# Performance work log

Hardware: AMD Instinct MI355X
Metric: run time of the kernel (lower is better)

Reference implementation:

```python
import jax, jax.numpy as jnp
import numpy as np

N = 100000
E = 800000
F_IN = 64
HID = 128


def setup_inputs() -> dict:
    key = jax.random.key(0)
    ks = jax.random.split(key, 10)
    x = jax.random.normal(ks[0], (N, F_IN), dtype=jnp.float32)
    edge_index = jax.random.randint(ks[1], (2, E), 0, N, dtype=jnp.int64)
    s = 0.05
    # PyG GraphConv: lin_rel (with bias) applied to aggregated neighbors, lin_root (no bias) to self
    return {
        "x": x,
        "edge_index": edge_index,
        "W1_rel": jax.random.normal(ks[2], (HID, F_IN), dtype=jnp.float32) * s,
        "b1": jnp.zeros((HID,), dtype=jnp.float32),
        "W1_root": jax.random.normal(ks[3], (HID, F_IN), dtype=jnp.float32) * s,
        "W2_rel": jax.random.normal(ks[4], (HID, HID), dtype=jnp.float32) * s,
        "b2": jnp.zeros((HID,), dtype=jnp.float32),
        "W2_root": jax.random.normal(ks[5], (HID, HID), dtype=jnp.float32) * s,
        "W_fc1": jax.random.normal(ks[6], (20, HID), dtype=jnp.float32) * s,
        "b_fc1": jnp.zeros((20,), dtype=jnp.float32),
        "W_fc2": jax.random.normal(ks[7], (1, 20), dtype=jnp.float32) * s,
        "b_fc2": jnp.zeros((1,), dtype=jnp.float32),
    }


def graph_conv(x, edge_index, W_rel, b_rel, W_root):
    # sum-aggregate source features onto destination nodes (PyG GraphConv, aggr='add')
    src, dst = edge_index[0], edge_index[1]
    agg = jax.ops.segment_sum(x[src], dst, num_segments=N)  # [N, F]
    return agg @ W_rel.T + b_rel + x @ W_root.T


def reference(x, edge_index, W1_rel, b1, W1_root, W2_rel, b2, W2_root,
              W_fc1, b_fc1, W_fc2, b_fc2):
    h = graph_conv(x, edge_index, W1_rel, b1, W1_root)
    h = jax.nn.elu(h)
    h = graph_conv(h, edge_index, W2_rel, b2, W2_root)
    h = jax.nn.relu(h @ W_fc1.T + b_fc1)
    out = h @ W_fc2.T + b_fc2  # [N, 1]
    return out
```

## Files before the change

### kernel.cpp

```cpp
#include <hip/hip_runtime.h>

#define N_NODES 100000
#define N_EDGES 800000
#define FIN 64
#define HID 128
#define NB1 391
#define SRCS_CAP (N_EDGES + 3 * N_NODES)
#define GI (1024 * 256)

typedef unsigned short ushort_t;
typedef __attribute__((ext_vector_type(8))) short short8;
typedef __attribute__((ext_vector_type(16))) float fx16;
typedef __attribute__((ext_vector_type(4))) unsigned short us4;

__device__ inline ushort_t f2bf(float f) {
    unsigned u = __float_as_uint(f);
    u += 0x7fffu + ((u >> 16) & 1u);
    return (ushort_t)(u >> 16);
}

__device__ inline void upadd(float* acc, uint4 A) {
    acc[0] += __uint_as_float(A.x << 16);
    acc[1] += __uint_as_float(A.x & 0xffff0000u);
    acc[2] += __uint_as_float(A.y << 16);
    acc[3] += __uint_as_float(A.y & 0xffff0000u);
    acc[4] += __uint_as_float(A.z << 16);
    acc[5] += __uint_as_float(A.z & 0xffff0000u);
    acc[6] += __uint_as_float(A.w << 16);
    acc[7] += __uint_as_float(A.w & 0xffff0000u);
}

__global__ __launch_bounds__(256) void init_kernel(
    const int* __restrict__ ei, const float* __restrict__ x,
    const float* __restrict__ W1rel, const float* __restrict__ W1root,
    const float* __restrict__ W2rel, const float* __restrict__ W2root,
    const float* __restrict__ b2, const float* __restrict__ Wfc1,
    const float* __restrict__ bfc1, const float* __restrict__ Wfc2,
    int* __restrict__ deg, int* __restrict__ flag, int* __restrict__ srcs,
    ushort_t* __restrict__ xb, ushort_t* __restrict__ Wb1,
    ushort_t* __restrict__ Mb, float* __restrict__ cbp, float* __restrict__ w2p) {
    __shared__ int s[256];
    int t = threadIdx.x;
    int gtid = blockIdx.x * 256 + t;

    if (gtid < N_NODES) deg[gtid] = 0;
    for (int k = gtid; k < SRCS_CAP; k += GI) srcs[k] = N_NODES;
    for (int i = gtid; i < N_NODES * FIN / 4; i += GI) {
        float4 v = ((const float4*)x)[i];
        us4 o = {f2bf(v.x), f2bf(v.y), f2bf(v.z), f2bf(v.w)};
        ((us4*)xb)[i] = o;
    }
    us4 z = {0, 0, 0, 0};
    if (gtid < 16) ((us4*)xb)[(size_t)N_NODES * 16 + gtid] = z;
    if (gtid < HID * HID) {
        int n = gtid >> 7, k = gtid & 127;
        float v = (k < FIN) ? W1rel[n * FIN + k] : W1root[n * FIN + (k - FIN)];
        Wb1[gtid] = f2bf(v);
    }
    if (blockIdx.x < 32) {
        int idx = blockIdx.x * 256 + t;
        int n = idx >> 7, k = idx & 127;
        float acc = 0.f;
        if (n < 20) {
            for (int j = 0; j < HID; j++) acc += Wfc1[n * HID + j] * W2rel[j * HID + k];
        } else if (n >= 32 && n < 52) {
            int m = n - 32;
            for (int j = 0; j < HID; j++) acc += Wfc1[m * HID + j] * W2root[j * HID + k];
        }
        Mb[idx] = f2bf(acc);
    }
    if (blockIdx.x == 32 && t < 32) {
        float cv = 0.f, wv = 0.f;
        if (t < 20) {
            for (int j = 0; j < HID; j++) cv += Wfc1[t * HID + j] * b2[j];
            cv += bfc1[t];
            wv = Wfc2[t];
        }
        cbp[t] = cv;
        w2p[t] = wv;
    }
    if (blockIdx.x == 33) {
        int bad = 0;
        for (int i = t; i < 8192; i += 256) bad |= ei[2 * i + 1];
        s[t] = bad;
        __syncthreads();
        for (int d = 128; d > 0; d >>= 1) {
            if (t < d) s[t] |= s[t + d];
            __syncthreads();
        }
        if (t == 0) *flag = (s[0] != 0) ? 1 : 0;
    }
}

__global__ void hist_kernel(const int* __restrict__ w, const int* __restrict__ flag,
                            int* __restrict__ deg) {
    int e = blockIdx.x * 256 + threadIdx.x;
    if (e >= N_EDGES) return;
    int is32 = *flag;
    int d = is32 ? w[N_EDGES + e] : w[2 * (N_EDGES + e)];
    atomicAdd(&deg[d], 1);
}

__global__ void scan1_kernel(const int* __restrict__ deg, int* __restrict__ off,
                             int* __restrict__ bsums) {
    __shared__ int s[256];
    int t = threadIdx.x;
    int i = blockIdx.x * 256 + t;
    int v = (i < N_NODES) ? ((deg[i] + 3) & ~3) : 0;
    s[t] = v;
    __syncthreads();
    for (int d = 1; d < 256; d <<= 1) {
        int w = (t >= d) ? s[t - d] : 0;
        __syncthreads();
        s[t] += w;
        __syncthreads();
    }
    if (i < N_NODES) off[i] = s[t] - v;
    if (t == 255) bsums[blockIdx.x] = s[255];
}

__global__ void scan23_kernel(int* __restrict__ off, const int* __restrict__ bsums,
                              int* __restrict__ cur) {
    __shared__ int s[256];
    int t = threadIdx.x, b = blockIdx.x;
    int pre = 0, tot = 0;
    for (int j = t; j < NB1; j += 256) {
        int v = bsums[j];
        if (j < b) pre += v;
        tot += v;
    }
    s[t] = pre;
    __syncthreads();
    for (int d = 128; d > 0; d >>= 1) {
        if (t < d) s[t] += s[t + d];
        __syncthreads();
    }
    int prefix = s[0];
    __syncthreads();
    int i = b * 256 + t;
    if (i < N_NODES) {
        int v = off[i] + prefix;
        off[i] = v;
        cur[i] = v;
    }
    if (b == 0) {
        s[t] = tot;
        __syncthreads();
        for (int d = 128; d > 0; d >>= 1) {
            if (t < d) s[t] += s[t + d];
            __syncthreads();
        }
        if (t == 0) off[N_NODES] = s[0];
    }
}

__global__ void scatter_kernel(const int* __restrict__ w, const int* __restrict__ flag,
                               int* __restrict__ cur, int* __restrict__ srcs) {
    int e = blockIdx.x * 256 + threadIdx.x;
    if (e >= N_EDGES) return;
    int is32 = *flag;
    int s = is32 ? w[e] : w[2 * e];
    int d = is32 ? w[N_EDGES + e] : w[2 * (N_EDGES + e)];
    int pos = atomicAdd(&cur[d], 1);
    srcs[pos] = s;
}

__global__ void agg1_kernel(const ushort_t* __restrict__ xb, const int* __restrict__ off,
                            const int* __restrict__ srcs, ushort_t* __restrict__ aggb) {
    int wid = (blockIdx.x * 256 + threadIdx.x) >> 6;
    int lane = threadIdx.x & 63;
    int n = lane >> 3;
    unsigned c = lane & 7;
    int node = wid * 8 + n;
    int b = off[node], e = off[node + 1];
    float acc[8];
#pragma unroll
    for (int j = 0; j < 8; j++) acc[j] = 0.f;
    const uint4* rows = (const uint4*)xb;
    for (int p = b; p < e; p += 4) {
        int4 s = *(const int4*)(srcs + p);
        uint4 A = rows[(unsigned)s.x * 8u + c];
        uint4 B = rows[(unsigned)s.y * 8u + c];
        uint4 C = rows[(unsigned)s.z * 8u + c];
        uint4 D = rows[(unsigned)s.w * 8u + c];
        upadd(acc, A);
        upadd(acc, B);
        upadd(acc, C);
        upadd(acc, D);
    }
    uint4 o = {(unsigned)f2bf(acc[0]) | ((unsigned)f2bf(acc[1]) << 16),
               (unsigned)f2bf(acc[2]) | ((unsigned)f2bf(acc[3]) << 16),
               (unsigned)f2bf(acc[4]) | ((unsigned)f2bf(acc[5]) << 16),
               (unsigned)f2bf(acc[6]) | ((unsigned)f2bf(acc[7]) << 16)};
    ((uint4*)(aggb + (size_t)node * FIN))[c] = o;
}

__global__ __launch_bounds__(256) void g12_kernel(
    const ushort_t* __restrict__ aggb, const ushort_t* __restrict__ xb,
    const ushort_t* __restrict__ Wb1, const float* __restrict__ b1,
    const ushort_t* __restrict__ Mb, ushort_t* __restrict__ uvb) {
    __shared__ ushort_t smem[24576];
    ushort_t* wl = smem;
    ushort_t* ml = smem + 16384;

    us4 z = {0, 0, 0, 0};
    if (blockIdx.x == 0 && threadIdx.x < 8)
        ((us4*)(uvb + (size_t)N_NODES * 64))[threadIdx.x] = z;

#pragma unroll
    for (int it = 0; it < 4; it++) {
        int q = it * 256 + threadIdx.x;
        int n = q >> 4, c = q & 15;
        short8 v = ((const short8*)Mb)[q];
        *(short8*)(ml + n * HID + ((c ^ (n & 7)) << 3)) = v;
    }
#pragma unroll
    for (int it = 0; it < 8; it++) {
        int q = it * 256 + threadIdx.x;
        int n = q >> 4, c = q & 15;
        short8 v = ((const short8*)Wb1)[q];
        *(short8*)(wl + n * HID + ((c ^ (n & 7)) << 3)) = v;
    }
    __syncthreads();

    int wave = threadIdx.x >> 6;
    int lane = threadIdx.x & 63;
    int half = lane >> 5, col = lane & 31;
    int nb = blockIdx.x * 128 + wave * 32;
    int nA = nb + col;
    if (nA >= N_NODES) nA = N_NODES - 1;

    short8 areg[8];
#pragma unroll
    for (int s = 0; s < 4; s++)
        areg[s] = *(const short8*)(aggb + (size_t)nA * FIN + s * 16 + half * 8);
#pragma unroll
    for (int s = 4; s < 8; s++)
        areg[s] = *(const short8*)(xb + (size_t)nA * FIN + (s - 4) * 16 + half * 8);

    fx16 acc[4];
#pragma unroll
    for (int jt = 0; jt < 4; jt++)
#pragma unroll
        for (int r = 0; r < 16; r++) acc[jt][r] = 0.f;

#pragma unroll
    for (int s = 0; s < 8; s++) {
        int c = 2 * s + half;
#pragma unroll
        for (int jt = 0; jt < 4; jt++) {
            int n = jt * 32 + col;
            short8 bq = *(const short8*)(wl + n * HID + ((c ^ (n & 7)) << 3));
            acc[jt] = __builtin_amdgcn_mfma_f32_32x32x16_bf16(areg[s], bq, acc[jt], 0, 0, 0);
        }
    }
    __syncthreads();

#pragma unroll
    for (int jt = 0; jt < 4; jt++) {
        int j = jt * 32 + col;
        float bias = b1[j];
#pragma unroll
        for (int r = 0; r < 16; r++) {
            int nl = wave * 32 + (r & 3) + 8 * (r >> 2) + 4 * half;
            float v = acc[jt][r] + bias;
            v = v > 0.f ? v : __expf(v) - 1.f;
            wl[nl * HID + (((j >> 3) ^ (nl & 7)) << 3) + (j & 7)] = f2bf(v);
        }
    }
    __syncthreads();

    int nl2 = wave * 32 + col;
    short8 af[8];
#pragma unroll
    for (int s = 0; s < 8; s++) {
        int c = 2 * s + half;
        af[s] = *(const short8*)(wl + nl2 * HID + ((c ^ (nl2 & 7)) << 3));
    }
    fx16 uacc[2];
#pragma unroll
    for (int jt = 0; jt < 2; jt++)
#pragma unroll
        for (int r = 0; r < 16; r++) uacc[jt][r] = 0.f;

#pragma unroll
    for (int s = 0; s < 8; s++) {
        int c = 2 * s + half;
#pragma unroll
        for (int jt = 0; jt < 2; jt++) {
            int n = jt * 32 + col;
            short8 bq = *(const short8*)(ml + n * HID + ((c ^ (n & 7)) << 3));
            uacc[jt] = __builtin_amdgcn_mfma_f32_32x32x16_bf16(af[s], bq, uacc[jt], 0, 0, 0);
        }
    }
#pragma unroll
    for (int jt = 0; jt < 2; jt++) {
        int j = jt * 32 + col;
#pragma unroll
        for (int r = 0; r < 16; r++) {
            int node = nb + (r & 3) + 8 * (r >> 2) + 4 * half;
            if (node < N_NODES) uvb[(size_t)node * 64 + j] = f2bf(uacc[jt][r]);
        }
    }
}

__global__ void agg3h_kernel(const ushort_t* __restrict__ uvb, const int* __restrict__ off,
                             const int* __restrict__ srcs, const float* __restrict__ cbp,
                             const float* __restrict__ w2p, const float* __restrict__ bfc2,
                             float* __restrict__ out) {
    int wid = (blockIdx.x * 256 + threadIdx.x) >> 6;
    int lane = threadIdx.x & 63;
    int n = lane >> 2;
    unsigned c = lane & 3;
    int node0 = wid * 16 + n;
    int node = (node0 < N_NODES) ? node0 : N_NODES - 1;
    int b = off[node], e = off[node + 1];
    float acc[8];
#pragma unroll
    for (int j = 0; j < 8; j++) acc[j] = 0.f;
    const uint4* rows = (const uint4*)uvb;
    for (int p = b; p < e; p += 4) {
        int4 s = *(const int4*)(srcs + p);
        uint4 A = rows[(unsigned)s.x * 8u + c];
        uint4 B = rows[(unsigned)s.y * 8u + c];
        uint4 C = rows[(unsigned)s.z * 8u + c];
        uint4 D = rows[(unsigned)s.w * 8u + c];
        upadd(acc, A);
        upadd(acc, B);
        upadd(acc, C);
        upadd(acc, D);
    }
    uint4 V = rows[(size_t)node * 8u + 4u + c];
    float vv[8];
    vv[0] = __uint_as_float(V.x << 16);
    vv[1] = __uint_as_float(V.x & 0xffff0000u);
    vv[2] = __uint_as_float(V.y << 16);
    vv[3] = __uint_as_float(V.y & 0xffff0000u);
    vv[4] = __uint_as_float(V.z << 16);
    vv[5] = __uint_as_float(V.z & 0xffff0000u);
    vv[6] = __uint_as_float(V.w << 16);
    vv[7] = __uint_as_float(V.w & 0xffff0000u);
    float4 cba = ((const float4*)cbp)[c * 2];
    float4 cbb = ((const float4*)cbp)[c * 2 + 1];
    float4 w2a = ((const float4*)w2p)[c * 2];
    float4 w2b = ((const float4*)w2p)[c * 2 + 1];
    float s = 0.f, a;
    a = acc[0] + vv[0] + cba.x; s += (a > 0.f ? a : 0.f) * w2a.x;
    a = acc[1] + vv[1] + cba.y; s += (a > 0.f ? a : 0.f) * w2a.y;
    a = acc[2] + vv[2] + cba.z; s += (a > 0.f ? a : 0.f) * w2a.z;
    a = acc[3] + vv[3] + cba.w; s += (a > 0.f ? a : 0.f) * w2a.w;
    a = acc[4] + vv[4] + cbb.x; s += (a > 0.f ? a : 0.f) * w2b.x;
    a = acc[5] + vv[5] + cbb.y; s += (a > 0.f ? a : 0.f) * w2b.y;
    a = acc[6] + vv[6] + cbb.z; s += (a > 0.f ? a : 0.f) * w2b.z;
    a = acc[7] + vv[7] + cbb.w; s += (a > 0.f ? a : 0.f) * w2b.w;
    s += __shfl_xor(s, 1);
    s += __shfl_xor(s, 2);
    if (c == 0 && node0 < N_NODES) out[node0] = s + bfc2[0];
}

extern "C" void kernel_launch(void* const* d_in, const int* in_sizes, int n_in,
                              void* d_out, int out_size, void* d_ws, size_t ws_size,
                              hipStream_t stream) {
    const float* x = (const float*)d_in[0];
    const int* ei = (const int*)d_in[1];
    const float* W1rel = (const float*)d_in[2];
    const float* b1 = (const float*)d_in[3];
    const float* W1root = (const float*)d_in[4];
    const float* W2rel = (const float*)d_in[5];
    const float* b2 = (const float*)d_in[6];
    const float* W2root = (const float*)d_in[7];
    const float* Wfc1 = (const float*)d_in[8];
    const float* bfc1 = (const float*)d_in[9];
    const float* Wfc2 = (const float*)d_in[10];
    const float* bfc2 = (const float*)d_in[11];
    float* out = (float*)d_out;

    char* ws = (char*)d_ws;
    size_t o = 0;
    auto alloc = [&](size_t bytes) {
        char* p = ws + o;
        o += (bytes + 255) & ~(size_t)255;
        return p;
    };
    int* deg = (int*)alloc((size_t)N_NODES * 4);
    int* off = (int*)alloc((size_t)(N_NODES + 1) * 4);
    int* bsums = (int*)alloc(4096);
    int* flag = (int*)alloc(256);
    int* cur = (int*)alloc((size_t)N_NODES * 4);
    int* srcs = (int*)alloc((size_t)SRCS_CAP * 4);
    ushort_t* xb = (ushort_t*)alloc((size_t)(N_NODES + 1) * FIN * 2);
    ushort_t* agg1b = (ushort_t*)alloc((size_t)N_NODES * FIN * 2);
    ushort_t* uvb = (ushort_t*)alloc((size_t)(N_NODES + 1) * 64 * 2);
    ushort_t* Wb1 = (ushort_t*)alloc((size_t)HID * HID * 2);
    ushort_t* Mb = (ushort_t*)alloc((size_t)64 * HID * 2);
    float* cbp = (float*)alloc(32 * 4);
    float* w2p = (float*)alloc(32 * 4);

    const int GW = (N_NODES + 127) / 128;
    const int GA1 = N_NODES / 32;
    const int GA3 = 1563;

    init_kernel<<<1024, 256, 0, stream>>>(ei, x, W1rel, W1root, W2rel, W2root,
                                          b2, Wfc1, bfc1, Wfc2,
                                          deg, flag, srcs, xb, Wb1, Mb, cbp, w2p);
    hist_kernel<<<(N_EDGES + 255) / 256, 256, 0, stream>>>(ei, flag, deg);
    scan1_kernel<<<NB1, 256, 0, stream>>>(deg, off, bsums);
    scan23_kernel<<<NB1, 256, 0, stream>>>(off, bsums, cur);
    scatter_kernel<<<(N_EDGES + 255) / 256, 256, 0, stream>>>(ei, flag, cur, srcs);
    agg1_kernel<<<GA1, 256, 0, stream>>>(xb, off, srcs, agg1b);
    g12_kernel<<<GW, 256, 0, stream>>>(agg1b, xb, Wb1, b1, Mb, uvb);
    agg3h_kernel<<<GA3, 256, 0, stream>>>(uvb, off, srcs, cbp, w2p, bfc2, out);
}
```

Baseline: 241.8 us.

## Replace scatter-phase atomics with histogram ranks and 4-way sub-bucketed counters

The histogram pass now records each edge's atomic rank and spreads counts across four sub-counters per node, chosen by edge index mod 4, to reduce atomic contention. The scan computes per-sub-bucket base offsets, so the scatter pass writes each source directly to base+rank with no atomics. The cost is extra memory traffic: a rank array of E ints, counter arrays four times larger, and more reads in the scans. Edge order within a node becomes deterministic up to the atomic order seen in the histogram.

```diff
diff --git a/kernel.cpp b/kernel.cpp
--- a/kernel.cpp
+++ b/kernel.cpp
@@ -36,14 +36,14 @@
     const float* __restrict__ W2rel, const float* __restrict__ W2root,
     const float* __restrict__ b2, const float* __restrict__ Wfc1,
     const float* __restrict__ bfc1, const float* __restrict__ Wfc2,
-    int* __restrict__ deg, int* __restrict__ flag, int* __restrict__ srcs,
+    int* __restrict__ deg4, int* __restrict__ flag, int* __restrict__ srcs,
     ushort_t* __restrict__ xb, ushort_t* __restrict__ Wb1,
     ushort_t* __restrict__ Mb, float* __restrict__ cbp, float* __restrict__ w2p) {
     __shared__ int s[256];
     int t = threadIdx.x;
     int gtid = blockIdx.x * 256 + t;
 
-    if (gtid < N_NODES) deg[gtid] = 0;
+    for (int k = gtid; k < 4 * N_NODES; k += GI) deg4[k] = 0;
     for (int k = gtid; k < SRCS_CAP; k += GI) srcs[k] = N_NODES;
     for (int i = gtid; i < N_NODES * FIN / 4; i += GI) {
         float4 v = ((const float4*)x)[i];
@@ -93,20 +93,24 @@
 }
 
 __global__ void hist_kernel(const int* __restrict__ w, const int* __restrict__ flag,
-                            int* __restrict__ deg) {
+                            int* __restrict__ deg4, int* __restrict__ rank) {
     int e = blockIdx.x * 256 + threadIdx.x;
     if (e >= N_EDGES) return;
     int is32 = *flag;
     int d = is32 ? w[N_EDGES + e] : w[2 * (N_EDGES + e)];
-    atomicAdd(&deg[d], 1);
-}
-
-__global__ void scan1_kernel(const int* __restrict__ deg, int* __restrict__ off,
+    rank[e] = atomicAdd(&deg4[(e & 3) * N_NODES + d], 1);
+}
+
+__global__ void scan1_kernel(const int* __restrict__ deg4, int* __restrict__ off,
                              int* __restrict__ bsums) {
     __shared__ int s[256];
     int t = threadIdx.x;
     int i = blockIdx.x * 256 + t;
-    int v = (i < N_NODES) ? ((deg[i] + 3) & ~3) : 0;
+    int v = 0;
+    if (i < N_NODES) {
+        int tot = deg4[i] + deg4[N_NODES + i] + deg4[2 * N_NODES + i] + deg4[3 * N_NODES + i];
+        v = (tot + 3) & ~3;
+    }
     s[t] = v;
     __syncthreads();
     for (int d = 1; d < 256; d <<= 1) {
@@ -120,7 +124,7 @@
 }
 
 __global__ void scan23_kernel(int* __restrict__ off, const int* __restrict__ bsums,
-                              int* __restrict__ cur) {
+                              const int* __restrict__ deg4, int* __restrict__ base4) {
     __shared__ int s[256];
     int t = threadIdx.x, b = blockIdx.x;
     int pre = 0, tot = 0;
@@ -141,7 +145,14 @@
     if (i < N_NODES) {
         int v = off[i] + prefix;
         off[i] = v;
-        cur[i] = v;
+        int b0 = v;
+        int b1 = b0 + deg4[i];
+        int b2 = b1 + deg4[N_NODES + i];
+        int b3 = b2 + deg4[2 * N_NODES + i];
+        base4[i] = b0;
+        base4[N_NODES + i] = b1;
+        base4[2 * N_NODES + i] = b2;
+        base4[3 * N_NODES + i] = b3;
     }
     if (b == 0) {
         s[t] = tot;
@@ -155,14 +166,14 @@
 }
 
 __global__ void scatter_kernel(const int* __restrict__ w, const int* __restrict__ flag,
-                               int* __restrict__ cur, int* __restrict__ srcs) {
+                               const int* __restrict__ base4, const int* __restrict__ rank,
+                               int* __restrict__ srcs) {
     int e = blockIdx.x * 256 + threadIdx.x;
     if (e >= N_EDGES) return;
     int is32 = *flag;
     int s = is32 ? w[e] : w[2 * e];
     int d = is32 ? w[N_EDGES + e] : w[2 * (N_EDGES + e)];
-    int pos = atomicAdd(&cur[d], 1);
-    srcs[pos] = s;
+    srcs[base4[(e & 3) * N_NODES + d] + rank[e]] = s;
 }
 
 __global__ void agg1_kernel(const ushort_t* __restrict__ xb, const int* __restrict__ off,
@@ -382,11 +393,12 @@
         o += (bytes + 255) & ~(size_t)255;
         return p;
     };
-    int* deg = (int*)alloc((size_t)N_NODES * 4);
+    int* deg4 = (int*)alloc((size_t)4 * N_NODES * 4);
     int* off = (int*)alloc((size_t)(N_NODES + 1) * 4);
     int* bsums = (int*)alloc(4096);
     int* flag = (int*)alloc(256);
-    int* cur = (int*)alloc((size_t)N_NODES * 4);
+    int* base4 = (int*)alloc((size_t)4 * N_NODES * 4);
+    int* rank = (int*)alloc((size_t)N_EDGES * 4);
     int* srcs = (int*)alloc((size_t)SRCS_CAP * 4);
     ushort_t* xb = (ushort_t*)alloc((size_t)(N_NODES + 1) * FIN * 2);
     ushort_t* agg1b = (ushort_t*)alloc((size_t)N_NODES * FIN * 2);
@@ -402,11 +414,11 @@
 
     init_kernel<<<1024, 256, 0, stream>>>(ei, x, W1rel, W1root, W2rel, W2root,
                                           b2, Wfc1, bfc1, Wfc2,
-                                          deg, flag, srcs, xb, Wb1, Mb, cbp, w2p);
-    hist_kernel<<<(N_EDGES + 255) / 256, 256, 0, stream>>>(ei, flag, deg);
-    scan1_kernel<<<NB1, 256, 0, stream>>>(deg, off, bsums);
-    scan23_kernel<<<NB1, 256, 0, stream>>>(off, bsums, cur);
-    scatter_kernel<<<(N_EDGES + 255) / 256, 256, 0, stream>>>(ei, flag, cur, srcs);
+                                          deg4, flag, srcs, xb, Wb1, Mb, cbp, w2p);
+    hist_kernel<<<(N_EDGES + 255) / 256, 256, 0, stream>>>(ei, flag, deg4, rank);
+    scan1_kernel<<<NB1, 256, 0, stream>>>(deg4, off, bsums);
+    scan23_kernel<<<NB1, 256, 0, stream>>>(off, bsums, deg4, base4);
+    scatter_kernel<<<(N_EDGES + 255) / 256, 256, 0, stream>>>(ei, flag, base4, rank, srcs);
     agg1_kernel<<<GA1, 256, 0, stream>>>(xb, off, srcs, agg1b);
     g12_kernel<<<GW, 256, 0, stream>>>(agg1b, xb, Wb1, b1, Mb, uvb);
     agg3h_kernel<<<GA3, 256, 0, stream>>>(uvb, off, srcs, cbp, w2p, bfc2, out);
```

New measurement: 203.6 us. 1.19x faster.
